# Optimization experiments

Measured on AMD Instinct MI355X. Metric: run time of the kernel, lower is better.

Reference implementation:

```python
import jax, jax.numpy as jnp
import numpy as np

N = 30000      # total nodes across batch
E = 480000     # edges (before self-loops)
B = 48         # graphs in batch
H = 4          # heads
D = 64         # hidden per head
NIN = 8
NOUT = 128
L = 10
SLOPE = 0.2    # GATConv default negative_slope


def setup_inputs() -> dict:
    key = jax.random.key(0)
    ks = jax.random.split(key, 12)
    s = 0.05
    x = jax.random.normal(ks[0], (N, NIN), jnp.float32)
    edge_index = jax.random.randint(ks[1], (2, E), 0, N, dtype=jnp.int32)
    batch = jnp.sort(jax.random.randint(ks[2], (N,), 0, B, dtype=jnp.int32))
    # layer 0 params (input dim NIN)
    W0 = jax.random.normal(ks[3], (NIN, H * D), jnp.float32) * s
    a_src0 = jax.random.normal(ks[4], (H, D), jnp.float32) * s
    a_dst0 = jax.random.normal(ks[5], (H, D), jnp.float32) * s
    b0 = jnp.zeros((H * D,), jnp.float32)
    # layers 1..L-1 (input dim H*D)
    Ws = jax.random.normal(ks[6], (L - 1, H * D, H * D), jnp.float32) * s
    a_srcs = jax.random.normal(ks[7], (L - 1, H, D), jnp.float32) * s
    a_dsts = jax.random.normal(ks[8], (L - 1, H, D), jnp.float32) * s
    bs = jnp.zeros((L - 1, H * D), jnp.float32)
    # readout head: GELU -> Linear(4*H*D -> NOUT)
    head_W = jax.random.normal(ks[9], (4 * H * D, NOUT), jnp.float32) * s
    head_b = jnp.zeros((NOUT,), jnp.float32)
    return dict(x=x, edge_index=edge_index, batch=batch,
                W0=W0, a_src0=a_src0, a_dst0=a_dst0, b0=b0,
                Ws=Ws, a_srcs=a_srcs, a_dsts=a_dsts, bs=bs,
                head_W=head_W, head_b=head_b)


def _gat_layer(x, W, a_src, a_dst, b, src, dst):
    n = x.shape[0]
    h = (x @ W).reshape(n, H, D)                      # [N,H,D]
    alpha_src = jnp.einsum('nhd,hd->nh', h, a_src)    # [N,H]
    alpha_dst = jnp.einsum('nhd,hd->nh', h, a_dst)
    e = jax.nn.leaky_relu(alpha_src[src] + alpha_dst[dst], SLOPE)  # [Etot,H]
    # segment softmax over destination neighborhoods
    m = jax.ops.segment_max(e, dst, num_segments=n)
    e = jnp.exp(e - m[dst])
    z = jax.ops.segment_sum(e, dst, num_segments=n)
    alpha = e / (z[dst] + 1e-16)                      # [Etot,H]
    msg = h[src] * alpha[:, :, None]                  # [Etot,H,D]
    out = jax.ops.segment_sum(msg, dst, num_segments=n)
    return out.reshape(n, H * D) + b


def reference(x, edge_index, batch, W0, a_src0, a_dst0, b0,
              Ws, a_srcs, a_dsts, bs, head_W, head_b):
    # add self loops (GATConv default add_self_loops=True)
    loops = jnp.arange(N, dtype=edge_index.dtype)
    src = jnp.concatenate([edge_index[0], loops])
    dst = jnp.concatenate([edge_index[1], loops])

    h = _gat_layer(x, W0, a_src0, a_dst0, b0, src, dst)
    for i in range(L - 1):
        h = jax.nn.gelu(h, approximate=False)  # dropout = identity (eval)
        h = _gat_layer(h, Ws[i], a_srcs[i], a_dsts[i], bs[i], src, dst)

    # MultiAggregation([min, max, mean, sum]) over graphs
    cnt = jax.ops.segment_sum(jnp.ones((N,), h.dtype), batch, num_segments=B)
    g_sum = jax.ops.segment_sum(h, batch, num_segments=B)
    g_mean = g_sum / jnp.maximum(cnt, 1.0)[:, None]
    g_min = jax.ops.segment_min(h, batch, num_segments=B)
    g_max = jax.ops.segment_max(h, batch, num_segments=B)
    g = jnp.concatenate([g_min, g_max, g_mean, g_sum], axis=-1)  # [B, 4*H*D]

    return jax.nn.gelu(g, approximate=False) @ head_W + head_b   # [B, NOUT]
```

## Files before the change

### kernel.cpp

```cpp
#include <hip/hip_runtime.h>
#include <math.h>

#define NN   30000
#define EE   480000
#define ETOT 510000
#define BB   48
#define HHH  4
#define DDD  64
#define CCH  256
#define NINP 8
#define NOUTP 128
#define NLAY 10
#define SLOPE 0.2f
#define PCHUNK 32

typedef short v8s  __attribute__((ext_vector_type(8)));
typedef float v4f  __attribute__((ext_vector_type(4)));

__device__ __forceinline__ float gelu_f(float x){
    return 0.5f * x * (1.0f + erff(x * 0.70710678118654752f));
}
__device__ __forceinline__ unsigned short f2bf(float f){
    unsigned u = __float_as_uint(f);
    unsigned r = u + 0x7FFF + ((u >> 16) & 1);
    return (unsigned short)(r >> 16);
}
__device__ __forceinline__ float bf2f(unsigned short b){
    return __uint_as_float(((unsigned)b) << 16);
}
__device__ __forceinline__ float lrelu(float e){
    return (e > 0.f) ? e : SLOPE * e;
}
__device__ __forceinline__ unsigned pack2(float a, float b){
    return (unsigned)f2bf(a) | ((unsigned)f2bf(b) << 16);
}
__device__ __forceinline__ float4 up4(uint2 u){
    float4 r;
    r.x = __uint_as_float(u.x << 16);
    r.y = __uint_as_float(u.x & 0xFFFF0000u);
    r.z = __uint_as_float(u.y << 16);
    r.w = __uint_as_float(u.y & 0xFFFF0000u);
    return r;
}

__global__ void count_k(const int* __restrict__ ei, int* __restrict__ cnt){
    int e = blockIdx.x * 256 + threadIdx.x;
    if (e >= ETOT) return;
    int d = (e < EE) ? ei[EE + e] : (e - EE);
    atomicAdd(&cnt[d], 1);
}

__global__ __launch_bounds__(1024) void scan_k(const int* __restrict__ cnt, int* __restrict__ row_ptr){
    const int PER = 30;
    int t = threadIdx.x;
    int base = t * PER;
    int v[PER];
    int sum = 0;
#pragma unroll
    for (int i = 0; i < PER; ++i){
        int x = (base + i < NN) ? cnt[base + i] : 0;
        v[i] = sum;
        sum += x;
    }
    int lane = t & 63, w = t >> 6;
    int inc = sum;
#pragma unroll
    for (int off = 1; off < 64; off <<= 1){
        int u = __shfl_up(inc, off);
        if (lane >= off) inc += u;
    }
    __shared__ int wtot[16], woff[16];
    if (lane == 63) wtot[w] = inc;
    __syncthreads();
    if (t == 0){
        int r = 0;
        for (int i = 0; i < 16; ++i){ woff[i] = r; r += wtot[i]; }
        row_ptr[NN] = r;
    }
    __syncthreads();
    int excl = woff[w] + (inc - sum);
#pragma unroll
    for (int i = 0; i < PER; ++i){
        if (base + i < NN) row_ptr[base + i] = excl + v[i];
    }
}

__global__ void scatter_k(const int* __restrict__ ei, const int* __restrict__ row_ptr,
                          int* __restrict__ cursor, int* __restrict__ csr_src){
    int e = blockIdx.x * 256 + threadIdx.x;
    if (e >= ETOT) return;
    int s, d;
    if (e < EE){ s = ei[e]; d = ei[EE + e]; } else { s = d = e - EE; }
    int pos = row_ptr[d] + atomicAdd(&cursor[d], 1);
    csr_src[pos] = s;
}

__global__ __launch_bounds__(256) void wconv_k(const float* __restrict__ Ws,
                                               unsigned short* __restrict__ WT_hi,
                                               unsigned short* __restrict__ WT_lo){
    __shared__ float tile[32][33];
    int l = blockIdx.x;
    int kt = (blockIdx.y >> 3) * 32;
    int nt = (blockIdx.y & 7) * 32;
    const float* W = Ws + (size_t)l * CCH * CCH;
    unsigned short* th = WT_hi + (size_t)l * CCH * CCH;
    unsigned short* tl = WT_lo + (size_t)l * CCH * CCH;
    int tx = threadIdx.x & 31, ty = threadIdx.x >> 5;
#pragma unroll
    for (int r = ty; r < 32; r += 8)
        tile[r][tx] = W[(size_t)(kt + r) * CCH + nt + tx];
    __syncthreads();
#pragma unroll
    for (int r = ty; r < 32; r += 8){
        float w = tile[tx][r];
        unsigned short h = f2bf(w);
        size_t o = (size_t)(nt + r) * CCH + kt + tx;
        th[o] = h;
        tl[o] = f2bf(w - bf2f(h));
    }
}

__global__ __launch_bounds__(256) void waconv_k(const float* __restrict__ Ws,
                                                const float* __restrict__ a_srcs,
                                                const float* __restrict__ a_dsts,
                                                unsigned short* __restrict__ wa_hi,
                                                unsigned short* __restrict__ wa_lo){
    int l = blockIdx.x;
    int j = blockIdx.y;
    int k = threadIdx.x;
    const float* W = Ws + (size_t)l * CCH * CCH;
    const float* av = (j < 4) ? (a_srcs + (size_t)l * CCH + j * DDD)
                              : (a_dsts + (size_t)l * CCH + (j - 4) * DDD);
    int cb = (j & 3) * DDD;
    float s = 0.f;
    const float4* wp = (const float4*)(W + (size_t)k * CCH + cb);
    const float4* ap = (const float4*)av;
#pragma unroll
    for (int d = 0; d < DDD / 4; ++d){
        float4 wv = wp[d], avv = ap[d];
        s += wv.x * avv.x + wv.y * avv.y + wv.z * avv.z + wv.w * avv.w;
    }
    unsigned short hb = f2bf(s);
    wa_hi[((size_t)l * 16 + j) * CCH + k] = hb;
    wa_lo[((size_t)l * 16 + j) * CCH + k] = f2bf(s - bf2f(hb));
    if (j >= 4){
        wa_hi[((size_t)l * 16 + j + 4) * CCH + k] = 0;
        wa_lo[((size_t)l * 16 + j + 4) * CCH + k] = 0;
        wa_hi[((size_t)l * 16 + j + 8) * CCH + k] = 0;
        wa_lo[((size_t)l * 16 + j + 8) * CCH + k] = 0;
    }
}

__global__ __launch_bounds__(256) void l0_fused(const float* __restrict__ x,
                                                const float* __restrict__ W0,
                                                const float* __restrict__ a_src,
                                                const float* __restrict__ a_dst,
                                                unsigned short* __restrict__ hout,
                                                float* __restrict__ asb,
                                                float* __restrict__ adb){
    __shared__ float xs[NINP];
    int n = blockIdx.x;
    int c = threadIdx.x;
    if (c < NINP) xs[c] = x[n * NINP + c];
    __syncthreads();
    float acc = 0.f;
#pragma unroll
    for (int k = 0; k < NINP; ++k) acc += xs[k] * W0[k * CCH + c];
    hout[(size_t)n * CCH + c] = f2bf(acc);
    int hh = c >> 6, lane = c & 63;
    float s1 = acc * a_src[hh * DDD + lane];
    float s2 = acc * a_dst[hh * DDD + lane];
#pragma unroll
    for (int off = 32; off; off >>= 1){
        s1 += __shfl_xor(s1, off);
        s2 += __shfl_xor(s2, off);
    }
    if (lane == 0){
        asb[(size_t)n * HHH + hh] = s1;
        adb[(size_t)n * HHH + hh] = s2;
    }
}

__global__ __launch_bounds__(256) void gemm_mfma(const unsigned short* __restrict__ A,
                                                 const unsigned short* __restrict__ Bhi,
                                                 const unsigned short* __restrict__ Blo,
                                                 const unsigned short* __restrict__ WAhi,
                                                 const unsigned short* __restrict__ WAlo,
                                                 unsigned short* __restrict__ C,
                                                 float* __restrict__ asb,
                                                 float* __restrict__ adb){
    int tid  = threadIdx.x;
    int lane = tid & 63, wave = tid >> 6;
    int wr = wave >> 1, wc = wave & 1;
    int rowBase = blockIdx.y * 128 + wr * 64;
    int colBase = blockIdx.x * 128 + wc * 64;
    int fr = lane & 15;
    int kg = lane >> 4;
    bool doAlpha = (blockIdx.x == 0) && (wc == 0);

    v4f acc[4][4];
#pragma unroll
    for (int mi = 0; mi < 4; ++mi)
#pragma unroll
        for (int ni = 0; ni < 4; ++ni) acc[mi][ni] = (v4f){0.f, 0.f, 0.f, 0.f};
    v4f acca[4];
#pragma unroll
    for (int mi = 0; mi < 4; ++mi) acca[mi] = (v4f){0.f, 0.f, 0.f, 0.f};

    const unsigned short* aptr[4];
#pragma unroll
    for (int mi = 0; mi < 4; ++mi){
        int r = rowBase + mi * 16 + fr;
        if (r >= NN) r = NN - 1;
        aptr[mi] = A + (size_t)r * CCH + kg * 8;
    }
    const unsigned short* bhp[4];
    const unsigned short* blp[4];
#pragma unroll
    for (int ni = 0; ni < 4; ++ni){
        int c = colBase + ni * 16 + fr;
        bhp[ni] = Bhi + (size_t)c * CCH + kg * 8;
        blp[ni] = Blo + (size_t)c * CCH + kg * 8;
    }
    const unsigned short* wahp = WAhi + (size_t)fr * CCH + kg * 8;
    const unsigned short* walp = WAlo + (size_t)fr * CCH + kg * 8;

    for (int kc = 0; kc < CCH; kc += 32){
        v8s a[4], bh[4], bl[4];
#pragma unroll
        for (int mi = 0; mi < 4; ++mi) a[mi] = *(const v8s*)(aptr[mi] + kc);
#pragma unroll
        for (int ni = 0; ni < 4; ++ni){
            bh[ni] = *(const v8s*)(bhp[ni] + kc);
            bl[ni] = *(const v8s*)(blp[ni] + kc);
        }
#pragma unroll
        for (int mi = 0; mi < 4; ++mi)
#pragma unroll
            for (int ni = 0; ni < 4; ++ni){
                acc[mi][ni] = __builtin_amdgcn_mfma_f32_16x16x32_bf16(a[mi], bh[ni], acc[mi][ni], 0, 0, 0);
                acc[mi][ni] = __builtin_amdgcn_mfma_f32_16x16x32_bf16(a[mi], bl[ni], acc[mi][ni], 0, 0, 0);
            }
        if (doAlpha){
            v8s wh = *(const v8s*)(wahp + kc);
            v8s wl = *(const v8s*)(walp + kc);
#pragma unroll
            for (int mi = 0; mi < 4; ++mi){
                acca[mi] = __builtin_amdgcn_mfma_f32_16x16x32_bf16(a[mi], wh, acca[mi], 0, 0, 0);
                acca[mi] = __builtin_amdgcn_mfma_f32_16x16x32_bf16(a[mi], wl, acca[mi], 0, 0, 0);
            }
        }
    }

#pragma unroll
    for (int mi = 0; mi < 4; ++mi)
#pragma unroll
        for (int j = 0; j < 4; ++j){
            int r = rowBase + mi * 16 + kg * 4 + j;
            if (r < NN){
#pragma unroll
                for (int ni = 0; ni < 4; ++ni)
                    C[(size_t)r * CCH + colBase + ni * 16 + fr] = f2bf(acc[mi][ni][j]);
            }
        }
    if (doAlpha){
#pragma unroll
        for (int mi = 0; mi < 4; ++mi)
#pragma unroll
            for (int j = 0; j < 4; ++j){
                int r = rowBase + mi * 16 + kg * 4 + j;
                if (r < NN){
                    float val = acca[mi][j];
                    if (fr < 4)      asb[(size_t)r * HHH + fr]       = val;
                    else if (fr < 8) adb[(size_t)r * HHH + (fr - 4)] = val;
                }
            }
    }
}

#define LOADG8(gg, U0, U1, U2, U3, A0, A1, A2, A3)                     \
    { int _b = (gg) << 3;                                              \
      int _e0 = _b + half, _e1 = _b + 2 + half;                        \
      int _e2 = _b + 4 + half, _e3 = _b + 6 + half;                    \
      int _i0 = ix_w[_e0], _i1 = ix_w[_e1];                            \
      int _i2 = ix_w[_e2], _i3 = ix_w[_e3];                            \
      A0 = al_w[_e0 * HHH + hc8];                                      \
      A1 = al_w[_e1 * HHH + hc8];                                      \
      A2 = al_w[_e2 * HHH + hc8];                                      \
      A3 = al_w[_e3 * HHH + hc8];                                      \
      U0 = *(const uint4*)(h + (size_t)_i0 * CCH + coff8);             \
      U1 = *(const uint4*)(h + (size_t)_i1 * CCH + coff8);             \
      U2 = *(const uint4*)(h + (size_t)_i2 * CCH + coff8);             \
      U3 = *(const uint4*)(h + (size_t)_i3 * CCH + coff8); }

#define CONSUME8(U0, U1, U2, U3, A0, A1, A2, A3)                       \
    { float4 _l0 = up4(make_uint2(U0.x, U0.y)), _h0 = up4(make_uint2(U0.z, U0.w)); \
      float4 _l1 = up4(make_uint2(U1.x, U1.y)), _h1 = up4(make_uint2(U1.z, U1.w)); \
      float4 _l2 = up4(make_uint2(U2.x, U2.y)), _h2 = up4(make_uint2(U2.z, U2.w)); \
      float4 _l3 = up4(make_uint2(U3.x, U3.y)), _h3 = up4(make_uint2(U3.z, U3.w)); \
      accLo.x += _l0.x * A0 + _l1.x * A1 + _l2.x * A2 + _l3.x * A3;    \
      accLo.y += _l0.y * A0 + _l1.y * A1 + _l2.y * A2 + _l3.y * A3;    \
      accLo.z += _l0.z * A0 + _l1.z * A1 + _l2.z * A2 + _l3.z * A3;    \
      accLo.w += _l0.w * A0 + _l1.w * A1 + _l2.w * A2 + _l3.w * A3;    \
      accHi.x += _h0.x * A0 + _h1.x * A1 + _h2.x * A2 + _h3.x * A3;    \
      accHi.y += _h0.y * A0 + _h1.y * A1 + _h2.y * A2 + _h3.y * A3;    \
      accHi.z += _h0.z * A0 + _h1.z * A1 + _h2.z * A2 + _h3.z * A3;    \
      accHi.w += _h0.w * A0 + _h1.w * A1 + _h2.w * A2 + _h3.w * A3; }

__global__ __launch_bounds__(256) void agg_k(const unsigned short* __restrict__ h,
                                             const float* __restrict__ asrc,
                                             const float* __restrict__ adst,
                                             const float* __restrict__ bias,
                                             const int* __restrict__ row_ptr,
                                             const int* __restrict__ csr_src,
                                             unsigned short* __restrict__ outg,
                                             float* __restrict__ outf,
                                             int mode){
    __shared__ float s_al[4][64 * HHH];
    __shared__ int   s_ix[4][64];

    int wave = threadIdx.x >> 6, lane = threadIdx.x & 63;
    int n = blockIdx.x * 4 + wave;
    int row0 = row_ptr[n];
    int deg  = row_ptr[n + 1] - row0;
    float4 ad = *(const float4*)(adst + (size_t)n * HHH);
    float* al_w = s_al[wave];
    int*   ix_w = s_ix[wave];

    if (deg <= 64){
        int k = lane;
        int s = 0;
        float x0 = 0.f, x1 = 0.f, x2 = 0.f, x3 = 0.f;
        if (k < deg){
            s = csr_src[row0 + k];
            float4 as = *(const float4*)(asrc + (size_t)s * HHH);
            x0 = __expf(lrelu(as.x + ad.x)); x1 = __expf(lrelu(as.y + ad.y));
            x2 = __expf(lrelu(as.z + ad.z)); x3 = __expf(lrelu(as.w + ad.w));
        }
        float z0 = x0, z1 = x1, z2 = x2, z3 = x3;
#pragma unroll
        for (int off = 32; off; off >>= 1){
            z0 += __shfl_xor(z0, off);
            z1 += __shfl_xor(z1, off);
            z2 += __shfl_xor(z2, off);
            z3 += __shfl_xor(z3, off);
        }
        if (k < deg){
            float4 alv;
            alv.x = x0 / (z0 + 1e-16f);
            alv.y = x1 / (z1 + 1e-16f);
            alv.z = x2 / (z2 + 1e-16f);
            alv.w = x3 / (z3 + 1e-16f);
            ix_w[k] = s;
            *(float4*)&al_w[k * HHH] = alv;
        }
        int half  = lane >> 5;
        int l32   = lane & 31;
        int coff8 = l32 << 3;
        int hc8   = l32 >> 3;
        float4 accLo = make_float4(0.f, 0.f, 0.f, 0.f);
        float4 accHi = make_float4(0.f, 0.f, 0.f, 0.f);

        int ng = deg >> 3;
        uint4 uA0, uA1, uA2, uA3, uB0, uB1, uB2, uB3;
        float aA0, aA1, aA2, aA3, aB0, aB1, aB2, aB3;
        if (ng > 0) LOADG8(0, uA0, uA1, uA2, uA3, aA0, aA1, aA2, aA3);
        if (ng > 1) LOADG8(1, uB0, uB1, uB2, uB3, aB0, aB1, aB2, aB3);
        for (int g = 0; g < ng; g += 2){
            if (g + 2 < ng) {
                CONSUME8(uA0, uA1, uA2, uA3, aA0, aA1, aA2, aA3);
                LOADG8(g + 2, uA0, uA1, uA2, uA3, aA0, aA1, aA2, aA3);
            } else {
                CONSUME8(uA0, uA1, uA2, uA3, aA0, aA1, aA2, aA3);
            }
            if (g + 1 < ng){
                if (g + 3 < ng) {
                    CONSUME8(uB0, uB1, uB2, uB3, aB0, aB1, aB2, aB3);
                    LOADG8(g + 3, uB0, uB1, uB2, uB3, aB0, aB1, aB2, aB3);
                } else {
                    CONSUME8(uB0, uB1, uB2, uB3, aB0, aB1, aB2, aB3);
                }
            }
        }
        for (int kk = ng << 3; kk < deg; kk += 2){
            int e = kk + half;
            if (e < deg){
                int i0 = ix_w[e];
                float a0 = al_w[e * HHH + hc8];
                uint4 u = *(const uint4*)(h + (size_t)i0 * CCH + coff8);
                float4 lo = up4(make_uint2(u.x, u.y)), hi = up4(make_uint2(u.z, u.w));
                accLo.x += lo.x * a0; accLo.y += lo.y * a0;
                accLo.z += lo.z * a0; accLo.w += lo.w * a0;
                accHi.x += hi.x * a0; accHi.y += hi.y * a0;
                accHi.z += hi.z * a0; accHi.w += hi.w * a0;
            }
        }
        accLo.x += __shfl_xor(accLo.x, 32); accLo.y += __shfl_xor(accLo.y, 32);
        accLo.z += __shfl_xor(accLo.z, 32); accLo.w += __shfl_xor(accLo.w, 32);
        accHi.x += __shfl_xor(accHi.x, 32); accHi.y += __shfl_xor(accHi.y, 32);
        accHi.z += __shfl_xor(accHi.z, 32); accHi.w += __shfl_xor(accHi.w, 32);
        if (half == 0){
            float4 b0v = *(const float4*)(bias + coff8);
            float4 b1v = *(const float4*)(bias + coff8 + 4);
            accLo.x += b0v.x; accLo.y += b0v.y; accLo.z += b0v.z; accLo.w += b0v.w;
            accHi.x += b1v.x; accHi.y += b1v.y; accHi.z += b1v.z; accHi.w += b1v.w;
            if (mode == 0){
                uint4 o;
                o.x = pack2(gelu_f(accLo.x), gelu_f(accLo.y));
                o.y = pack2(gelu_f(accLo.z), gelu_f(accLo.w));
                o.z = pack2(gelu_f(accHi.x), gelu_f(accHi.y));
                o.w = pack2(gelu_f(accHi.z), gelu_f(accHi.w));
                *(uint4*)(outg + (size_t)n * CCH + coff8) = o;
            } else {
                *(float4*)(outf + (size_t)n * CCH + coff8)     = accLo;
                *(float4*)(outf + (size_t)n * CCH + coff8 + 4) = accHi;
            }
        }
        return;
    }

    int coff = lane << 2;
    int hc   = lane >> 4;
    float4 acc = make_float4(0.f, 0.f, 0.f, 0.f);
    float m0 = -INFINITY, m1 = -INFINITY, m2 = -INFINITY, m3 = -INFINITY;
    float z0 = 0.f, z1 = 0.f, z2 = 0.f, z3 = 0.f;
    for (int c0 = 0; c0 < deg; c0 += 64){
        int k = c0 + lane;
        float e0 = -INFINITY, e1 = -INFINITY, e2 = -INFINITY, e3 = -INFINITY;
        if (k < deg){
            int s = csr_src[row0 + k];
            float4 as = *(const float4*)(asrc + (size_t)s * HHH);
            e0 = lrelu(as.x + ad.x); e1 = lrelu(as.y + ad.y);
            e2 = lrelu(as.z + ad.z); e3 = lrelu(as.w + ad.w);
        }
        float c0m = e0, c1m = e1, c2m = e2, c3m = e3;
#pragma unroll
        for (int off = 32; off; off >>= 1){
            c0m = fmaxf(c0m, __shfl_xor(c0m, off));
            c1m = fmaxf(c1m, __shfl_xor(c1m, off));
            c2m = fmaxf(c2m, __shfl_xor(c2m, off));
            c3m = fmaxf(c3m, __shfl_xor(c3m, off));
        }
        float n0 = fmaxf(m0, c0m), n1 = fmaxf(m1, c1m);
        float n2 = fmaxf(m2, c2m), n3 = fmaxf(m3, c3m);
        float x0 = 0.f, x1 = 0.f, x2 = 0.f, x3 = 0.f;
        if (k < deg){
            x0 = __expf(e0 - n0); x1 = __expf(e1 - n1);
            x2 = __expf(e2 - n2); x3 = __expf(e3 - n3);
        }
        float s0 = x0, s1 = x1, s2 = x2, s3 = x3;
#pragma unroll
        for (int off = 32; off; off >>= 1){
            s0 += __shfl_xor(s0, off);
            s1 += __shfl_xor(s1, off);
            s2 += __shfl_xor(s2, off);
            s3 += __shfl_xor(s3, off);
        }
        z0 = z0 * ((m0 == -INFINITY) ? 0.f : __expf(m0 - n0)) + s0;
        z1 = z1 * ((m1 == -INFINITY) ? 0.f : __expf(m1 - n1)) + s1;
        z2 = z2 * ((m2 == -INFINITY) ? 0.f : __expf(m2 - n2)) + s2;
        z3 = z3 * ((m3 == -INFINITY) ? 0.f : __expf(m3 - n3)) + s3;
        m0 = n0; m1 = n1; m2 = n2; m3 = n3;
    }
    float iz0 = 1.f / (z0 + 1e-16f), iz1 = 1.f / (z1 + 1e-16f);
    float iz2 = 1.f / (z2 + 1e-16f), iz3 = 1.f / (z3 + 1e-16f);
    for (int c0 = 0; c0 < deg; c0 += 64){
        int k = c0 + lane;
        if (k < deg){
            int s = csr_src[row0 + k];
            float4 as = *(const float4*)(asrc + (size_t)s * HHH);
            float4 alv;
            alv.x = __expf(lrelu(as.x + ad.x) - m0) * iz0;
            alv.y = __expf(lrelu(as.y + ad.y) - m1) * iz1;
            alv.z = __expf(lrelu(as.z + ad.z) - m2) * iz2;
            alv.w = __expf(lrelu(as.w + ad.w) - m3) * iz3;
            ix_w[lane] = s;
            *(float4*)&al_w[lane * HHH] = alv;
        }
        int cnt = deg - c0; if (cnt > 64) cnt = 64;
        for (int j = 0; j < cnt; ++j){
            int i0 = ix_w[j];
            float a0 = al_w[j * HHH + hc];
            float4 v0 = up4(*(const uint2*)(h + (size_t)i0 * CCH + coff));
            acc.x += v0.x * a0; acc.y += v0.y * a0; acc.z += v0.z * a0; acc.w += v0.w * a0;
        }
    }
    float4 bv = *(const float4*)(bias + coff);
    acc.x += bv.x; acc.y += bv.y; acc.z += bv.z; acc.w += bv.w;
    if (mode == 0){
        uint2 o;
        o.x = pack2(gelu_f(acc.x), gelu_f(acc.y));
        o.y = pack2(gelu_f(acc.z), gelu_f(acc.w));
        *(uint2*)(outg + (size_t)n * CCH + coff) = o;
    } else {
        *(float4*)(outf + (size_t)n * CCH + coff) = acc;
    }
}

__global__ void gptr_k(const int* __restrict__ batch, int* __restrict__ gptr){
    int i = blockIdx.x * 256 + threadIdx.x;
    if (i >= NN) return;
    int bi = batch[i];
    int bp = (i == 0) ? -1 : batch[i - 1];
    for (int g = bp + 1; g <= bi; ++g) gptr[g] = i;
    if (i == NN - 1){
        for (int g = bi + 1; g <= BB; ++g) gptr[g] = NN;
    }
}

__global__ __launch_bounds__(256) void pool1_k(const float* __restrict__ h,
                                               const int* __restrict__ gptr,
                                               float* __restrict__ part){
    const int S1 = BB * PCHUNK * CCH;
    int b = blockIdx.x, j = blockIdx.y, c = threadIdx.x;
    int s = gptr[b], e = gptr[b + 1];
    int len = e - s;
    int per = (len + PCHUNK - 1) / PCHUNK;
    int r0 = s + j * per;
    int r1 = r0 + per; if (r1 > e) r1 = e;
    float mn = INFINITY, mx = -INFINITY, sm = 0.f;
    int n = r0;
    for (; n + 4 <= r1; n += 4){
        float v0 = h[(size_t)(n + 0) * CCH + c];
        float v1 = h[(size_t)(n + 1) * CCH + c];
        float v2 = h[(size_t)(n + 2) * CCH + c];
        float v3 = h[(size_t)(n + 3) * CCH + c];
        mn = fminf(mn, fminf(fminf(v0, v1), fminf(v2, v3)));
        mx = fmaxf(mx, fmaxf(fmaxf(v0, v1), fmaxf(v2, v3)));
        sm += (v0 + v1) + (v2 + v3);
    }
    for (; n < r1; ++n){
        float v = h[(size_t)n * CCH + c];
        mn = fminf(mn, v); mx = fmaxf(mx, v); sm += v;
    }
    size_t o = ((size_t)b * PCHUNK + j) * CCH + c;
    part[o] = mn; part[S1 + o] = mx; part[2 * (size_t)S1 + o] = sm;
}

__global__ __launch_bounds__(256) void pool2_k(const float* __restrict__ part,
                                               const int* __restrict__ gptr,
                                               float* __restrict__ gbuf){
    const int S1 = BB * PCHUNK * CCH;
    int b = blockIdx.x, c = threadIdx.x;
    float mn = INFINITY, mx = -INFINITY, sm = 0.f;
#pragma unroll
    for (int j = 0; j < PCHUNK; ++j){
        size_t o = ((size_t)b * PCHUNK + j) * CCH + c;
        mn = fminf(mn, part[o]);
        mx = fmaxf(mx, part[S1 + o]);
        sm += part[2 * (size_t)S1 + o];
    }
    int cnt = gptr[b + 1] - gptr[b];
    float mean = sm / fmaxf((float)cnt, 1.0f);
    if (cnt == 0){ mn = 0.f; mx = 0.f; }
    gbuf[b * 4 * CCH + 0 * CCH + c] = mn;
    gbuf[b * 4 * CCH + 1 * CCH + c] = mx;
    gbuf[b * 4 * CCH + 2 * CCH + c] = mean;
    gbuf[b * 4 * CCH + 3 * CCH + c] = sm;
}

__global__ __launch_bounds__(128) void head_k(const float* __restrict__ gbuf,
                                              const float* __restrict__ head_W,
                                              const float* __restrict__ head_b,
                                              float* __restrict__ out){
    __shared__ float gs[4 * CCH];
    int b = blockIdx.x;
    int o = threadIdx.x;
    for (int k = o; k < 4 * CCH; k += 128) gs[k] = gelu_f(gbuf[b * 4 * CCH + k]);
    __syncthreads();
    float acc = head_b[o];
    for (int k = 0; k < 4 * CCH; ++k) acc += gs[k] * head_W[k * NOUTP + o];
    out[b * NOUTP + o] = acc;
}

extern "C" void kernel_launch(void* const* d_in, const int* in_sizes, int n_in,
                              void* d_out, int out_size, void* d_ws, size_t ws_size,
                              hipStream_t stream){
    const float* x        = (const float*)d_in[0];
    const int*   ei       = (const int*)  d_in[1];
    const int*   batch    = (const int*)  d_in[2];
    const float* W0       = (const float*)d_in[3];
    const float* a_src0   = (const float*)d_in[4];
    const float* a_dst0   = (const float*)d_in[5];
    const float* b0       = (const float*)d_in[6];
    const float* Ws       = (const float*)d_in[7];
    const float* a_srcs   = (const float*)d_in[8];
    const float* a_dsts   = (const float*)d_in[9];
    const float* bs       = (const float*)d_in[10];
    const float* head_W   = (const float*)d_in[11];
    const float* head_b   = (const float*)d_in[12];
    float* out = (float*)d_out;

    char* p = (char*)d_ws;
    float* buf0f = (float*)p;                   p += (size_t)NN * CCH * 4;
    unsigned short* buf0g = (unsigned short*)p; p += (size_t)NN * CCH * 2;
    unsigned short* buf1  = (unsigned short*)p; p += (size_t)NN * CCH * 2;
    float* asb  = (float*)p;                   p += (size_t)NN * HHH * 4;
    float* adb  = (float*)p;                   p += (size_t)NN * HHH * 4;
    int* row_ptr = (int*)p;                    p += 120016;
    int* cnt     = (int*)p;                    p += (size_t)NN * 4;
    int* csr_src = (int*)p;                    p += (size_t)ETOT * 4;
    float* gbuf  = (float*)p;                  p += (size_t)BB * 4 * CCH * 4;
    int* gptr    = (int*)p;                    p += 208;
    unsigned short* wthi = (unsigned short*)p; p += (size_t)(NLAY - 1) * CCH * CCH * 2;
    unsigned short* wtlo = (unsigned short*)p; p += (size_t)(NLAY - 1) * CCH * CCH * 2;
    unsigned short* wahi = (unsigned short*)p; p += (size_t)(NLAY - 1) * 16 * CCH * 2;
    unsigned short* walo = (unsigned short*)p; p += (size_t)(NLAY - 1) * 16 * CCH * 2;
    float* pscr = (float*)p;                   p += (size_t)3 * BB * PCHUNK * CCH * 4;

    hipMemsetAsync(cnt, 0, (size_t)NN * 4, stream);
    count_k<<<(ETOT + 255) / 256, 256, 0, stream>>>(ei, cnt);
    scan_k<<<1, 1024, 0, stream>>>(cnt, row_ptr);
    hipMemsetAsync(cnt, 0, (size_t)NN * 4, stream);
    scatter_k<<<(ETOT + 255) / 256, 256, 0, stream>>>(ei, row_ptr, cnt, csr_src);
    gptr_k<<<(NN + 255) / 256, 256, 0, stream>>>(batch, gptr);
    wconv_k<<<dim3(NLAY - 1, 64), 256, 0, stream>>>(Ws, wthi, wtlo);
    waconv_k<<<dim3(NLAY - 1, 8), 256, 0, stream>>>(Ws, a_srcs, a_dsts, wahi, walo);

    l0_fused<<<NN, 256, 0, stream>>>(x, W0, a_src0, a_dst0, buf1, asb, adb);
    agg_k<<<NN / 4, 256, 0, stream>>>(buf1, asb, adb, b0, row_ptr, csr_src,
                                      buf0g, buf0f, 0);

    dim3 ggrid(2, (NN + 127) / 128);
    for (int l = 1; l < NLAY; ++l){
        const unsigned short* whl = wthi + (size_t)(l - 1) * CCH * CCH;
        const unsigned short* wll = wtlo + (size_t)(l - 1) * CCH * CCH;
        const unsigned short* wal_h = wahi + (size_t)(l - 1) * 16 * CCH;
        const unsigned short* wal_l = walo + (size_t)(l - 1) * 16 * CCH;
        const float* bl  = bs + (size_t)(l - 1) * CCH;
        gemm_mfma<<<ggrid, 256, 0, stream>>>(buf0g, whl, wll, wal_h, wal_l, buf1, asb, adb);
        agg_k<<<NN / 4, 256, 0, stream>>>(buf1, asb, adb, bl, row_ptr, csr_src,
                                          buf0g, buf0f, (l == NLAY - 1) ? 1 : 0);
    }

    dim3 pgrid(BB, PCHUNK);
    pool1_k<<<pgrid, 256, 0, stream>>>(buf0f, gptr, pscr);
    pool2_k<<<BB, 256, 0, stream>>>(pscr, gptr, gbuf);
    head_k<<<BB, 128, 0, stream>>>(gbuf, head_W, head_b, out);
}
```

Baseline: 945.5 us.

## Shrink GEMM tiles, grid-stride layer-0 kernel, pad aggregation edges to multiples of eight

The MFMA GEMM tile drops from 128x128 to 64 rows by 128 columns, with each wave owning 32 columns. This doubles the number of blocks to fill more compute units and cuts register pressure, at the cost of loading B more often. The layer-0 kernel becomes a grid-stride loop over 512 blocks, so W0 and the attention vectors are loaded once per thread rather than once per node. In aggregation, each neighbourhood's edges are padded to a multiple of eight with zero-weight self entries, which removes the scalar tail loop but adds some wasted loads.

```diff
diff --git a/kernel.cpp b/kernel.cpp
--- a/kernel.cpp
+++ b/kernel.cpp
@@ -159,25 +159,32 @@
                                                 float* __restrict__ asb,
                                                 float* __restrict__ adb){
     __shared__ float xs[NINP];
-    int n = blockIdx.x;
     int c = threadIdx.x;
-    if (c < NINP) xs[c] = x[n * NINP + c];
-    __syncthreads();
-    float acc = 0.f;
-#pragma unroll
-    for (int k = 0; k < NINP; ++k) acc += xs[k] * W0[k * CCH + c];
-    hout[(size_t)n * CCH + c] = f2bf(acc);
+    float w0[NINP];
+#pragma unroll
+    for (int k = 0; k < NINP; ++k) w0[k] = W0[k * CCH + c];
     int hh = c >> 6, lane = c & 63;
-    float s1 = acc * a_src[hh * DDD + lane];
-    float s2 = acc * a_dst[hh * DDD + lane];
-#pragma unroll
-    for (int off = 32; off; off >>= 1){
-        s1 += __shfl_xor(s1, off);
-        s2 += __shfl_xor(s2, off);
-    }
-    if (lane == 0){
-        asb[(size_t)n * HHH + hh] = s1;
-        adb[(size_t)n * HHH + hh] = s2;
+    float asv = a_src[hh * DDD + lane];
+    float adv = a_dst[hh * DDD + lane];
+    for (int n = blockIdx.x; n < NN; n += gridDim.x){
+        if (c < NINP) xs[c] = x[n * NINP + c];
+        __syncthreads();
+        float acc = 0.f;
+#pragma unroll
+        for (int k = 0; k < NINP; ++k) acc += xs[k] * w0[k];
+        hout[(size_t)n * CCH + c] = f2bf(acc);
+        float s1 = acc * asv;
+        float s2 = acc * adv;
+#pragma unroll
+        for (int off = 32; off; off >>= 1){
+            s1 += __shfl_xor(s1, off);
+            s2 += __shfl_xor(s2, off);
+        }
+        if (lane == 0){
+            asb[(size_t)n * HHH + hh] = s1;
+            adb[(size_t)n * HHH + hh] = s2;
+        }
+        __syncthreads();
     }
 }
 
@@ -191,18 +198,17 @@
                                                  float* __restrict__ adb){
     int tid  = threadIdx.x;
     int lane = tid & 63, wave = tid >> 6;
-    int wr = wave >> 1, wc = wave & 1;
-    int rowBase = blockIdx.y * 128 + wr * 64;
-    int colBase = blockIdx.x * 128 + wc * 64;
+    int rowBase = blockIdx.y * 64;
+    int colBase = blockIdx.x * 128 + wave * 32;
     int fr = lane & 15;
     int kg = lane >> 4;
-    bool doAlpha = (blockIdx.x == 0) && (wc == 0);
-
-    v4f acc[4][4];
+    bool doAlpha = (blockIdx.x == 0) && (wave == 0);
+
+    v4f acc[4][2];
 #pragma unroll
     for (int mi = 0; mi < 4; ++mi)
 #pragma unroll
-        for (int ni = 0; ni < 4; ++ni) acc[mi][ni] = (v4f){0.f, 0.f, 0.f, 0.f};
+        for (int ni = 0; ni < 2; ++ni) acc[mi][ni] = (v4f){0.f, 0.f, 0.f, 0.f};
     v4f acca[4];
 #pragma unroll
     for (int mi = 0; mi < 4; ++mi) acca[mi] = (v4f){0.f, 0.f, 0.f, 0.f};
@@ -214,10 +220,10 @@
         if (r >= NN) r = NN - 1;
         aptr[mi] = A + (size_t)r * CCH + kg * 8;
     }
-    const unsigned short* bhp[4];
-    const unsigned short* blp[4];
-#pragma unroll
-    for (int ni = 0; ni < 4; ++ni){
+    const unsigned short* bhp[2];
+    const unsigned short* blp[2];
+#pragma unroll
+    for (int ni = 0; ni < 2; ++ni){
         int c = colBase + ni * 16 + fr;
         bhp[ni] = Bhi + (size_t)c * CCH + kg * 8;
         blp[ni] = Blo + (size_t)c * CCH + kg * 8;
@@ -226,18 +232,18 @@
     const unsigned short* walp = WAlo + (size_t)fr * CCH + kg * 8;
 
     for (int kc = 0; kc < CCH; kc += 32){
-        v8s a[4], bh[4], bl[4];
+        v8s a[4], bh[2], bl[2];
 #pragma unroll
         for (int mi = 0; mi < 4; ++mi) a[mi] = *(const v8s*)(aptr[mi] + kc);
 #pragma unroll
-        for (int ni = 0; ni < 4; ++ni){
+        for (int ni = 0; ni < 2; ++ni){
             bh[ni] = *(const v8s*)(bhp[ni] + kc);
             bl[ni] = *(const v8s*)(blp[ni] + kc);
         }
 #pragma unroll
         for (int mi = 0; mi < 4; ++mi)
 #pragma unroll
-            for (int ni = 0; ni < 4; ++ni){
+            for (int ni = 0; ni < 2; ++ni){
                 acc[mi][ni] = __builtin_amdgcn_mfma_f32_16x16x32_bf16(a[mi], bh[ni], acc[mi][ni], 0, 0, 0);
                 acc[mi][ni] = __builtin_amdgcn_mfma_f32_16x16x32_bf16(a[mi], bl[ni], acc[mi][ni], 0, 0, 0);
             }
@@ -259,7 +265,7 @@
             int r = rowBase + mi * 16 + kg * 4 + j;
             if (r < NN){
 #pragma unroll
-                for (int ni = 0; ni < 4; ++ni)
+                for (int ni = 0; ni < 2; ++ni)
                     C[(size_t)r * CCH + colBase + ni * 16 + fr] = f2bf(acc[mi][ni][j]);
             }
         }
@@ -329,6 +335,7 @@
 
     if (deg <= 64){
         int k = lane;
+        int padDeg = (deg + 7) & ~7;
         int s = 0;
         float x0 = 0.f, x1 = 0.f, x2 = 0.f, x3 = 0.f;
         if (k < deg){
@@ -353,6 +360,9 @@
             alv.w = x3 / (z3 + 1e-16f);
             ix_w[k] = s;
             *(float4*)&al_w[k * HHH] = alv;
+        } else if (k < padDeg){
+            ix_w[k] = n;
+            *(float4*)&al_w[k * HHH] = make_float4(0.f, 0.f, 0.f, 0.f);
         }
         int half  = lane >> 5;
         int l32   = lane & 31;
@@ -361,7 +371,7 @@
         float4 accLo = make_float4(0.f, 0.f, 0.f, 0.f);
         float4 accHi = make_float4(0.f, 0.f, 0.f, 0.f);
 
-        int ng = deg >> 3;
+        int ng = padDeg >> 3;
         uint4 uA0, uA1, uA2, uA3, uB0, uB1, uB2, uB3;
         float aA0, aA1, aA2, aA3, aB0, aB1, aB2, aB3;
         if (ng > 0) LOADG8(0, uA0, uA1, uA2, uA3, aA0, aA1, aA2, aA3);
@@ -380,19 +390,6 @@
                 } else {
                     CONSUME8(uB0, uB1, uB2, uB3, aB0, aB1, aB2, aB3);
                 }
-            }
-        }
-        for (int kk = ng << 3; kk < deg; kk += 2){
-            int e = kk + half;
-            if (e < deg){
-                int i0 = ix_w[e];
-                float a0 = al_w[e * HHH + hc8];
-                uint4 u = *(const uint4*)(h + (size_t)i0 * CCH + coff8);
-                float4 lo = up4(make_uint2(u.x, u.y)), hi = up4(make_uint2(u.z, u.w));
-                accLo.x += lo.x * a0; accLo.y += lo.y * a0;
-                accLo.z += lo.z * a0; accLo.w += lo.w * a0;
-                accHi.x += hi.x * a0; accHi.y += hi.y * a0;
-                accHi.z += hi.z * a0; accHi.w += hi.w * a0;
             }
         }
         accLo.x += __shfl_xor(accLo.x, 32); accLo.y += __shfl_xor(accLo.y, 32);
@@ -617,11 +614,11 @@
     wconv_k<<<dim3(NLAY - 1, 64), 256, 0, stream>>>(Ws, wthi, wtlo);
     waconv_k<<<dim3(NLAY - 1, 8), 256, 0, stream>>>(Ws, a_srcs, a_dsts, wahi, walo);
 
-    l0_fused<<<NN, 256, 0, stream>>>(x, W0, a_src0, a_dst0, buf1, asb, adb);
+    l0_fused<<<512, 256, 0, stream>>>(x, W0, a_src0, a_dst0, buf1, asb, adb);
     agg_k<<<NN / 4, 256, 0, stream>>>(buf1, asb, adb, b0, row_ptr, csr_src,
                                       buf0g, buf0f, 0);
 
-    dim3 ggrid(2, (NN + 127) / 128);
+    dim3 ggrid(2, (NN + 63) / 64);
     for (int l = 1; l < NLAY; ++l){
         const unsigned short* whl = wthi + (size_t)(l - 1) * CCH * CCH;
         const unsigned short* wll = wtlo + (size_t)(l - 1) * CCH * CCH;
```

After: 990.0 us. 1.05x slower.
